# Optimization experiments

Measured on AMD Instinct MI355X. Metric: run time of the kernel, lower is better.

Reference implementation:

```python
import jax, jax.numpy as jnp
import numpy as np

N = 100000   # nodes
E = 1600000  # edges
F = 128      # input node features
H = 128      # hidden channels
G = 512      # graphs in batch
EPS = 1e-5   # BatchNorm eps


def setup_inputs() -> dict:
    key = jax.random.key(0)
    ks = jax.random.split(key, 24)
    x = jax.random.normal(ks[0], (N, F), jnp.float32)
    edge_index = jax.random.randint(ks[1], (2, E), 0, N)
    batch = jnp.sort(jax.random.randint(ks[2], (N,), 0, G))

    def lin_w(k, i, o):
        return jax.random.normal(k, (i, o), jnp.float32) / np.sqrt(i)

    inp = {
        "x": x, "edge_index": edge_index, "batch": batch,
        "W1": lin_w(ks[3], F, H), "b1": jnp.zeros((H,), jnp.float32),
        "g1": jnp.ones((H,), jnp.float32), "be1": jnp.zeros((H,), jnp.float32),
        "m1": 0.1 * jax.random.normal(ks[4], (H,), jnp.float32),
        "v1": jax.random.uniform(ks[5], (H,), jnp.float32) + 0.5,
        "W2": lin_w(ks[6], H, H), "b2": jnp.zeros((H,), jnp.float32),
        "g2": jnp.ones((H,), jnp.float32), "be2": jnp.zeros((H,), jnp.float32),
        "m2": 0.1 * jax.random.normal(ks[7], (H,), jnp.float32),
        "v2": jax.random.uniform(ks[8], (H,), jnp.float32) + 0.5,
        "W3": lin_w(ks[9], H, H), "b3": jnp.zeros((H,), jnp.float32),
        "g3": jnp.ones((H,), jnp.float32), "be3": jnp.zeros((H,), jnp.float32),
        "m3": 0.1 * jax.random.normal(ks[10], (H,), jnp.float32),
        "v3": jax.random.uniform(ks[11], (H,), jnp.float32) + 0.5,
        "Wl": lin_w(ks[12], H, 1), "bl": jnp.zeros((1,), jnp.float32),
    }
    return inp


def _gcn_norm(edge_index):
    # add self-loops, then symmetric normalization deg^-1/2 A_hat deg^-1/2
    loops = jnp.arange(N)
    src = jnp.concatenate([edge_index[0], loops])
    dst = jnp.concatenate([edge_index[1], loops])
    deg = jax.ops.segment_sum(jnp.ones_like(src, jnp.float32), dst, num_segments=N)
    dinv = jax.lax.rsqrt(jnp.maximum(deg, 1.0))
    norm = dinv[src] * dinv[dst]  # [E+N]
    return src, dst, norm


def _gcn_conv(x, W, b, src, dst, norm):
    h = x @ W                                    # [N,H] dense GEMM first (PyG order)
    msg = h[src] * norm[:, None]                 # gather + scale, [E+N,H]
    agg = jax.ops.segment_sum(msg, dst, num_segments=N)  # scatter-add
    return agg + b


def _bn_relu(x, g, be, m, v):
    # inference BatchNorm1d (running stats) + ReLU
    return jax.nn.relu((x - m) * jax.lax.rsqrt(v + EPS) * g + be)


def reference(x, edge_index, batch,
              W1, b1, g1, be1, m1, v1,
              W2, b2, g2, be2, m2, v2,
              W3, b3, g3, be3, m3, v3,
              Wl, bl):
    src, dst, norm = _gcn_norm(edge_index)
    h = _bn_relu(_gcn_conv(x, W1, b1, src, dst, norm), g1, be1, m1, v1)
    h = _bn_relu(_gcn_conv(h, W2, b2, src, dst, norm), g2, be2, m2, v2)
    h = _bn_relu(_gcn_conv(h, W3, b3, src, dst, norm), g3, be3, m3, v3)
    # global mean pool over graphs
    sums = jax.ops.segment_sum(h, batch, num_segments=G)           # [G,H]
    cnt = jax.ops.segment_sum(jnp.ones((N,), jnp.float32), batch, num_segments=G)
    pooled = sums / jnp.maximum(cnt, 1.0)[:, None]
    # dropout is identity at inference; final linear
    return pooled @ Wl + bl  # [G,1]
```

## Files before the change

kernel.cpp:

```cpp
#include <hip/hip_runtime.h>
#include <hip/hip_bf16.h>

#define NN 100000
#define NE 1600000
#define HD 128
#define NG 512
#define BN_EPS 1e-5f

#define GEMM_BLOCKS 1563

typedef __attribute__((ext_vector_type(8))) short short8;
typedef __attribute__((ext_vector_type(4))) float floatx4;

__device__ __forceinline__ ushort f2bf(float f) {
    union { float f; uint u; } v; v.f = f;
    uint r = (v.u + 0x7FFF + ((v.u >> 16) & 1)) >> 16;
    return (ushort)r;
}
__device__ __forceinline__ float bflo(uint u) { union { uint u; float f; } v; v.u = u << 16; return v.f; }
__device__ __forceinline__ float bfhi(uint u) { union { uint u; float f; } v; v.u = u & 0xFFFF0000u; return v.f; }

__global__ void k_zero_i(int* p, int n) {
    int i = blockIdx.x * 256 + threadIdx.x;
    if (i < n) p[i] = 0;
}

__global__ void k_prep_all(const float* __restrict__ W1, const float* __restrict__ W2,
                           const float* __restrict__ W3,
                           ushort* __restrict__ Wt1, ushort* __restrict__ Wt2,
                           ushort* __restrict__ Wt3,
                           const float* __restrict__ b1, const float* __restrict__ g1,
                           const float* __restrict__ be1, const float* __restrict__ m1,
                           const float* __restrict__ v1,
                           const float* __restrict__ b2, const float* __restrict__ g2,
                           const float* __restrict__ be2, const float* __restrict__ m2,
                           const float* __restrict__ v2,
                           const float* __restrict__ b3, const float* __restrict__ g3,
                           const float* __restrict__ be3, const float* __restrict__ m3,
                           const float* __restrict__ v3,
                           float* scale1, float* shift1, float* scale2, float* shift2,
                           float* scale3, float* shift3,
                           const int* __restrict__ batch, int* __restrict__ gstart) {
    int blk = blockIdx.x, tid = threadIdx.x;
    if (blk < 192) {
        int w = blk >> 6;
        int i = (blk & 63) * 256 + tid;
        const float* W = (w == 0) ? W1 : (w == 1) ? W2 : W3;
        ushort* Wt = (w == 0) ? Wt1 : (w == 1) ? Wt2 : Wt3;
        int k = i >> 7, n = i & 127;
        Wt[n * 128 + k] = f2bf(W[i]);
    } else if (blk < 195) {
        if (tid >= 128) return;
        int l = blk - 192;
        const float *b, *g, *be, *m, *v;
        float *sc, *sh;
        if (l == 0)      { b = b1; g = g1; be = be1; m = m1; v = v1; sc = scale1; sh = shift1; }
        else if (l == 1) { b = b2; g = g2; be = be2; m = m2; v = v2; sc = scale2; sh = shift2; }
        else             { b = b3; g = g3; be = be3; m = m3; v = v3; sc = scale3; sh = shift3; }
        float s = g[tid] * rsqrtf(v[tid] + BN_EPS);
        sc[tid] = s;
        sh[tid] = (b[tid] - m[tid]) * s + be[tid];
    } else {
        int g = (blk - 195) * 256 + tid;
        if (g > NG) return;
        if (g == NG) { gstart[NG] = NN; return; }
        int lo = 0, hi = NN;
        while (lo < hi) {
            int mid = (lo + hi) >> 1;
            if (batch[mid] < g) lo = mid + 1; else hi = mid;
        }
        gstart[g] = lo;
    }
}

__global__ void k_hist_rank(const int* __restrict__ dst, int* __restrict__ indeg,
                            int* __restrict__ rank) {
    int e = blockIdx.x * 256 + threadIdx.x;
    if (e < NE) rank[e] = atomicAdd(&indeg[dst[e]], 1);
}

__launch_bounds__(256)
__global__ void k_gemm1(const float* __restrict__ x, const ushort* __restrict__ Wt,
                        ushort* __restrict__ hs) {
    const int tid = threadIdx.x;
    const int wave = tid >> 6, lane = tid & 63;
    const int m = lane & 15, kg = lane >> 4;
    const long row0 = (long)blockIdx.x * 64 + wave * 16;

    long arow = row0 + m;
    long arc = arow < NN ? arow : (NN - 1);
    const float* xf = x + arc * 128;
    short8 a[4];
#pragma unroll
    for (int s = 0; s < 4; ++s) {
        float4 f0 = *(const float4*)(xf + s * 32 + kg * 8);
        float4 f1 = *(const float4*)(xf + s * 32 + kg * 8 + 4);
        short8 t;
        t[0] = (short)f2bf(f0.x); t[1] = (short)f2bf(f0.y);
        t[2] = (short)f2bf(f0.z); t[3] = (short)f2bf(f0.w);
        t[4] = (short)f2bf(f1.x); t[5] = (short)f2bf(f1.y);
        t[6] = (short)f2bf(f1.z); t[7] = (short)f2bf(f1.w);
        a[s] = t;
    }

    floatx4 acc[8];
#pragma unroll
    for (int ct = 0; ct < 8; ++ct) acc[ct] = (floatx4){0.f, 0.f, 0.f, 0.f};

#pragma unroll
    for (int s = 0; s < 4; ++s) {
#pragma unroll
        for (int ct = 0; ct < 8; ++ct) {
            short8 b = *(const short8*)(Wt + (ct * 16 + m) * 128 + s * 32 + kg * 8);
            acc[ct] = __builtin_amdgcn_mfma_f32_16x16x32_bf16(a[s], b, acc[ct], 0, 0, 0);
        }
    }

#pragma unroll
    for (int r = 0; r < 4; ++r) {
        long orow = row0 + kg * 4 + r;
        if (orow < NN) {
#pragma unroll
            for (int ct = 0; ct < 8; ++ct)
                hs[orow * 128 + ct * 16 + m] = f2bf(acc[ct][r]);
        }
    }
}

__global__ void k_scan1d(const int* __restrict__ indeg, int* __restrict__ rs,
                         int* __restrict__ aux, float* __restrict__ dinv) {
    __shared__ int s[256];
    int t = threadIdx.x;
    int base = blockIdx.x * 1024 + t * 4;
    int v0 = 0, v1 = 0, v2 = 0, v3 = 0;
    if (base + 0 < NN) v0 = indeg[base + 0];
    if (base + 1 < NN) v1 = indeg[base + 1];
    if (base + 2 < NN) v2 = indeg[base + 2];
    if (base + 3 < NN) v3 = indeg[base + 3];
    if (base + 0 < NN) dinv[base + 0] = rsqrtf((float)(v0 + 1));
    if (base + 1 < NN) dinv[base + 1] = rsqrtf((float)(v1 + 1));
    if (base + 2 < NN) dinv[base + 2] = rsqrtf((float)(v2 + 1));
    if (base + 3 < NN) dinv[base + 3] = rsqrtf((float)(v3 + 1));
    int tsum = v0 + v1 + v2 + v3;
    s[t] = tsum;
    __syncthreads();
    for (int o = 1; o < 256; o <<= 1) {
        int x = 0;
        if (t >= o) x = s[t - o];
        __syncthreads();
        s[t] += x;
        __syncthreads();
    }
    int excl = s[t] - tsum;
    if (base + 0 < NN) rs[base + 0] = excl;
    if (base + 1 < NN) rs[base + 1] = excl + v0;
    if (base + 2 < NN) rs[base + 2] = excl + v0 + v1;
    if (base + 3 < NN) rs[base + 3] = excl + v0 + v1 + v2;
    if (t == 255) aux[blockIdx.x] = s[255];
}

__global__ void k_scan2(int* __restrict__ aux, int nblk) {
    __shared__ int s[128];
    int t = threadIdx.x;
    int v = (t < nblk) ? aux[t] : 0;
    s[t] = v;
    __syncthreads();
    for (int o = 1; o < 128; o <<= 1) {
        int x = 0;
        if (t >= o) x = s[t - o];
        __syncthreads();
        s[t] += x;
        __syncthreads();
    }
    if (t < nblk) aux[t] = s[t] - v;
}

__global__ void k_scan3(int* __restrict__ rs, const int* __restrict__ aux) {
    int i = blockIdx.x * 256 + threadIdx.x;
    if (i < NN) rs[i] += aux[i >> 10];
    if (i == 0) rs[NN] = NE;
}

__global__ void k_fill(const int* __restrict__ src, const int* __restrict__ dst,
                       const int* __restrict__ rank, const int* __restrict__ rs,
                       int* __restrict__ csr) {
    int e = blockIdx.x * 256 + threadIdx.x;
    if (e >= NE) return;
    csr[rs[dst[e]] + rank[e]] = src[e];
}

#define WT_STRIDE 136
__launch_bounds__(256)
__global__ void k_gemm_l23(const ushort* __restrict__ xb, const ushort* __restrict__ Wt,
                           const float* __restrict__ dinv, ushort* __restrict__ hs) {
    __shared__ ushort sWt[128 * WT_STRIDE];
    const int tid = threadIdx.x;
    for (int i = tid; i < 2048; i += 256) {
        int row = i >> 4, seg = i & 15;
        *(uint4*)&sWt[row * WT_STRIDE + seg * 8] = *(const uint4*)(Wt + row * 128 + seg * 8);
    }
    __syncthreads();

    const int wave = tid >> 6, lane = tid & 63;
    const int m = lane & 15, kg = lane >> 4;
    const long row0 = (long)blockIdx.x * 64 + wave * 16;

    long arow = row0 + m;
    long arc = arow < NN ? arow : (NN - 1);
    short8 a[4];
#pragma unroll
    for (int s = 0; s < 4; ++s)
        a[s] = *(const short8*)(xb + arc * 128 + s * 32 + kg * 8);

    floatx4 acc[8];
#pragma unroll
    for (int ct = 0; ct < 8; ++ct) acc[ct] = (floatx4){0.f, 0.f, 0.f, 0.f};

#pragma unroll
    for (int s = 0; s < 4; ++s) {
#pragma unroll
        for (int ct = 0; ct < 8; ++ct) {
            short8 b = *(const short8*)&sWt[(ct * 16 + m) * WT_STRIDE + s * 32 + kg * 8];
            acc[ct] = __builtin_amdgcn_mfma_f32_16x16x32_bf16(a[s], b, acc[ct], 0, 0, 0);
        }
    }

#pragma unroll
    for (int r = 0; r < 4; ++r) {
        long orow = row0 + kg * 4 + r;
        if (orow < NN) {
            float dd = dinv[orow];
#pragma unroll
            for (int ct = 0; ct < 8; ++ct)
                hs[orow * 128 + ct * 16 + m] = f2bf(acc[ct][r] * dd);
        }
    }
}

template <bool SCALE_SRC>
__global__ void k_gather_bf(const ushort* __restrict__ hs, const int* __restrict__ rs,
                            const int* __restrict__ csr, const float* __restrict__ dinv,
                            const float* __restrict__ scale, const float* __restrict__ shift,
                            ushort* __restrict__ xout) {
    int t = blockIdx.x * 256 + threadIdx.x;
    int d = t >> 4;
    if (d >= NN) return;
    int lane = t & 15;
    int c0 = lane * 8;
    int e0 = rs[d], e1 = rs[d + 1];
    float dd = dinv[d];

    uint4 sv = *(const uint4*)(hs + (long)d * 128 + c0);
    float w = SCALE_SRC ? dd : 1.0f;
    float a0 = w * bflo(sv.x), a1 = w * bfhi(sv.x), a2 = w * bflo(sv.y), a3 = w * bfhi(sv.y);
    float a4 = w * bflo(sv.z), a5 = w * bfhi(sv.z), a6 = w * bflo(sv.w), a7 = w * bfhi(sv.w);

    int j = e0;
    for (; j + 1 < e1; j += 2) {
        int s0 = csr[j], s1 = csr[j + 1];
        uint4 v0 = *(const uint4*)(hs + (long)s0 * 128 + c0);
        uint4 v1 = *(const uint4*)(hs + (long)s1 * 128 + c0);
        if (SCALE_SRC) {
            float w0 = dinv[s0], w1 = dinv[s1];
            a0 += w0 * bflo(v0.x) + w1 * bflo(v1.x);
            a1 += w0 * bfhi(v0.x) + w1 * bfhi(v1.x);
            a2 += w0 * bflo(v0.y) + w1 * bflo(v1.y);
            a3 += w0 * bfhi(v0.y) + w1 * bfhi(v1.y);
            a4 += w0 * bflo(v0.z) + w1 * bflo(v1.z);
            a5 += w0 * bfhi(v0.z) + w1 * bfhi(v1.z);
            a6 += w0 * bflo(v0.w) + w1 * bflo(v1.w);
            a7 += w0 * bfhi(v0.w) + w1 * bfhi(v1.w);
        } else {
            a0 += bflo(v0.x) + bflo(v1.x); a1 += bfhi(v0.x) + bfhi(v1.x);
            a2 += bflo(v0.y) + bflo(v1.y); a3 += bfhi(v0.y) + bfhi(v1.y);
            a4 += bflo(v0.z) + bflo(v1.z); a5 += bfhi(v0.z) + bfhi(v1.z);
            a6 += bflo(v0.w) + bflo(v1.w); a7 += bfhi(v0.w) + bfhi(v1.w);
        }
    }
    if (j < e1) {
        int s0 = csr[j];
        uint4 v0 = *(const uint4*)(hs + (long)s0 * 128 + c0);
        float w0 = SCALE_SRC ? dinv[s0] : 1.0f;
        a0 += w0 * bflo(v0.x); a1 += w0 * bfhi(v0.x);
        a2 += w0 * bflo(v0.y); a3 += w0 * bfhi(v0.y);
        a4 += w0 * bflo(v0.z); a5 += w0 * bfhi(v0.z);
        a6 += w0 * bflo(v0.w); a7 += w0 * bfhi(v0.w);
    }

    float4 sca = *(const float4*)(scale + c0);
    float4 scb = *(const float4*)(scale + c0 + 4);
    float4 sha = *(const float4*)(shift + c0);
    float4 shb = *(const float4*)(shift + c0 + 4);
    float r0 = fmaxf(dd * a0 * sca.x + sha.x, 0.f);
    float r1 = fmaxf(dd * a1 * sca.y + sha.y, 0.f);
    float r2 = fmaxf(dd * a2 * sca.z + sha.z, 0.f);
    float r3 = fmaxf(dd * a3 * sca.w + sha.w, 0.f);
    float r4 = fmaxf(dd * a4 * scb.x + shb.x, 0.f);
    float r5 = fmaxf(dd * a5 * scb.y + shb.y, 0.f);
    float r6 = fmaxf(dd * a6 * scb.z + shb.z, 0.f);
    float r7 = fmaxf(dd * a7 * scb.w + shb.w, 0.f);
    uint4 o;
    o.x = (uint)f2bf(r0) | ((uint)f2bf(r1) << 16);
    o.y = (uint)f2bf(r2) | ((uint)f2bf(r3) << 16);
    o.z = (uint)f2bf(r4) | ((uint)f2bf(r5) << 16);
    o.w = (uint)f2bf(r6) | ((uint)f2bf(r7) << 16);
    *(uint4*)(xout + (long)d * 128 + c0) = o;
}

__global__ void k_pool_final2(const ushort* __restrict__ x, const int* __restrict__ gstart,
                              const float* __restrict__ Wl, const float* __restrict__ bl,
                              float* __restrict__ out) {
    __shared__ float red[256];
    int g = blockIdx.x;
    int tid = threadIdx.x;
    int f = tid & 127;
    int half = tid >> 7;
    int i0 = gstart[g], i1 = gstart[g + 1];

    float acc = 0.f;
    for (int i = i0 + half; i < i1; i += 2) {
        union { uint u; float f; } v; v.u = (uint)x[(long)i * 128 + f] << 16;
        acc += v.f;
    }
    red[tid] = acc;
    __syncthreads();
    if (tid < 128) red[tid] = (red[tid] + red[tid + 128]) * Wl[tid];
    __syncthreads();
    for (int o = 64; o > 0; o >>= 1) {
        if (tid < o) red[tid] += red[tid + o];
        __syncthreads();
    }
    if (tid == 0) out[g] = red[0] / fmaxf((float)(i1 - i0), 1.f) + bl[0];
}

extern "C" void kernel_launch(void* const* d_in, const int* in_sizes, int n_in,
                              void* d_out, int out_size, void* d_ws, size_t ws_size,
                              hipStream_t stream) {
    const float* x   = (const float*)d_in[0];
    const int*   ei  = (const int*)d_in[1];
    const int*   bat = (const int*)d_in[2];
    const float* W1  = (const float*)d_in[3];
    const float* b1  = (const float*)d_in[4];
    const float* g1  = (const float*)d_in[5];
    const float* be1 = (const float*)d_in[6];
    const float* m1  = (const float*)d_in[7];
    const float* v1  = (const float*)d_in[8];
    const float* W2  = (const float*)d_in[9];
    const float* b2  = (const float*)d_in[10];
    const float* g2  = (const float*)d_in[11];
    const float* be2 = (const float*)d_in[12];
    const float* m2  = (const float*)d_in[13];
    const float* v2  = (const float*)d_in[14];
    const float* W3  = (const float*)d_in[15];
    const float* b3  = (const float*)d_in[16];
    const float* g3  = (const float*)d_in[17];
    const float* be3 = (const float*)d_in[18];
    const float* m3  = (const float*)d_in[19];
    const float* v3  = (const float*)d_in[20];
    const float* Wl  = (const float*)d_in[21];
    const float* bl  = (const float*)d_in[22];
    float* out = (float*)d_out;

    const int* srcp = ei;
    const int* dstp = ei + NE;

    char* ws = (char*)d_ws;
    size_t off = 0;
    auto alloc = [&](size_t bytes) { char* p = ws + off; off += (bytes + 255) & ~255ULL; return p; };
    float*  dinv   = (float*) alloc(NN * 4);
    int*    indeg  = (int*)   alloc(NN * 4);
    int*    rs     = (int*)   alloc((NN + 1) * 4);
    int*    aux    = (int*)   alloc(128 * 4);
    int*    csr    = (int*)   alloc(NE * 4);
    int*    rank   = (int*)   alloc(NE * 4);
    float*  scale1 = (float*) alloc(HD * 4);
    float*  shift1 = (float*) alloc(HD * 4);
    float*  scale2 = (float*) alloc(HD * 4);
    float*  shift2 = (float*) alloc(HD * 4);
    float*  scale3 = (float*) alloc(HD * 4);
    float*  shift3 = (float*) alloc(HD * 4);
    int*    gstart = (int*)   alloc((NG + 1) * 4);
    ushort* Wt1    = (ushort*)alloc(128 * 128 * 2);
    ushort* Wt2    = (ushort*)alloc(128 * 128 * 2);
    ushort* Wt3    = (ushort*)alloc(128 * 128 * 2);
    ushort* hs     = (ushort*)alloc((size_t)NN * HD * 2);
    ushort* xbuf   = (ushort*)alloc((size_t)NN * HD * 2);

    const int nblk_scan = (NN + 1023) / 1024;
    const int grid_n    = (NN + 255) / 256;
    const int grid_e    = (NE + 255) / 256;
    const int gath_grid = (NN * 16 + 255) / 256;

    k_zero_i<<<grid_n, 256, 0, stream>>>(indeg, NN);
    k_prep_all<<<198, 256, 0, stream>>>(W1, W2, W3, Wt1, Wt2, Wt3,
                                        b1, g1, be1, m1, v1,
                                        b2, g2, be2, m2, v2,
                                        b3, g3, be3, m3, v3,
                                        scale1, shift1, scale2, shift2, scale3, shift3,
                                        bat, gstart);

    k_hist_rank<<<grid_e, 256, 0, stream>>>(dstp, indeg, rank);
    k_gemm1<<<GEMM_BLOCKS, 256, 0, stream>>>(x, Wt1, hs);

    k_scan1d<<<nblk_scan, 256, 0, stream>>>(indeg, rs, aux, dinv);
    k_scan2<<<1, 128, 0, stream>>>(aux, nblk_scan);
    k_scan3<<<grid_n, 256, 0, stream>>>(rs, aux);
    k_fill<<<grid_e, 256, 0, stream>>>(srcp, dstp, rank, rs, csr);

    k_gather_bf<true><<<gath_grid, 256, 0, stream>>>(hs, rs, csr, dinv, scale1, shift1, xbuf);
    k_gemm_l23<<<GEMM_BLOCKS, 256, 0, stream>>>(xbuf, Wt2, dinv, hs);
    k_gather_bf<false><<<gath_grid, 256, 0, stream>>>(hs, rs, csr, dinv, scale2, shift2, xbuf);
    k_gemm_l23<<<GEMM_BLOCKS, 256, 0, stream>>>(xbuf, Wt3, dinv, hs);
    k_gather_bf<false><<<gath_grid, 256, 0, stream>>>(hs, rs, csr, dinv, scale3, shift3, xbuf);

    k_pool_final2<<<NG, 256, 0, stream>>>(xbuf, gstart, Wl, bl, out);
}
```

Baseline: 520.0 us.

## Partition degree histogram by XCD with workgroup-scope atomics and chunk cursors

The in-degree histogram is restructured so that each XCD (read from the hardware XCC_ID register) owns a contiguous 1/8 range of destination nodes. Every XCD scans all edges through a per-XCD work-stealing chunk cursor and applies only the increments that fall in its range, using workgroup-scope atomics so they can resolve in the local L2 rather than going device-wide. The separate zeroing kernel is folded into the prep kernel, which saves one launch. In exchange each XCD reads the whole dst array (8x read traffic), and correctness depends on each XCD's L2 staying coherent for its own partition and on the assumption that blocks get scheduled onto all 8 XCDs.

```diff
diff --git a/kernel.cpp b/kernel.cpp
--- a/kernel.cpp
+++ b/kernel.cpp
@@ -8,6 +8,10 @@
 #define BN_EPS 1e-5f
 
 #define GEMM_BLOCKS 1563
+#define NXCD 8
+#define NODES_PER_XCD (NN / NXCD)
+#define CHUNK 4096
+#define NCHUNK ((NE + CHUNK - 1) / CHUNK)
 
 typedef __attribute__((ext_vector_type(8))) short short8;
 typedef __attribute__((ext_vector_type(4))) float floatx4;
@@ -20,9 +24,14 @@
 __device__ __forceinline__ float bflo(uint u) { union { uint u; float f; } v; v.u = u << 16; return v.f; }
 __device__ __forceinline__ float bfhi(uint u) { union { uint u; float f; } v; v.u = u & 0xFFFF0000u; return v.f; }
 
-__global__ void k_zero_i(int* p, int n) {
-    int i = blockIdx.x * 256 + threadIdx.x;
-    if (i < n) p[i] = 0;
+__device__ __forceinline__ uint xcc_id() {
+    uint x;
+    asm volatile("s_getreg_b32 %0, hwreg(HW_REG_XCC_ID)" : "=s"(x));
+    return x & 7u;
+}
+
+__device__ __forceinline__ int atomAddL2(int* p, int v) {
+    return __hip_atomic_fetch_add(p, v, __ATOMIC_RELAXED, __HIP_MEMORY_SCOPE_WORKGROUP);
 }
 
 __global__ void k_prep_all(const float* __restrict__ W1, const float* __restrict__ W2,
@@ -40,7 +49,8 @@
                            const float* __restrict__ v3,
                            float* scale1, float* shift1, float* scale2, float* shift2,
                            float* scale3, float* shift3,
-                           const int* __restrict__ batch, int* __restrict__ gstart) {
+                           const int* __restrict__ batch, int* __restrict__ gstart,
+                           int* __restrict__ indeg, int* __restrict__ cursor) {
     int blk = blockIdx.x, tid = threadIdx.x;
     if (blk < 192) {
         int w = blk >> 6;
@@ -60,7 +70,7 @@
         float s = g[tid] * rsqrtf(v[tid] + BN_EPS);
         sc[tid] = s;
         sh[tid] = (b[tid] - m[tid]) * s + be[tid];
-    } else {
+    } else if (blk < 198) {
         int g = (blk - 195) * 256 + tid;
         if (g > NG) return;
         if (g == NG) { gstart[NG] = NN; return; }
@@ -70,13 +80,48 @@
             if (batch[mid] < g) lo = mid + 1; else hi = mid;
         }
         gstart[g] = lo;
-    }
-}
-
-__global__ void k_hist_rank(const int* __restrict__ dst, int* __restrict__ indeg,
-                            int* __restrict__ rank) {
-    int e = blockIdx.x * 256 + threadIdx.x;
-    if (e < NE) rank[e] = atomicAdd(&indeg[dst[e]], 1);
+    } else {
+        int i = (blk - 198) * 256 + tid;
+        if (i < NN) indeg[i] = 0;
+        if (blk == 198 && tid < NXCD) cursor[tid] = 0;
+    }
+}
+
+__launch_bounds__(256)
+__global__ void k_hist_x(const int* __restrict__ dst, int* __restrict__ indeg,
+                         int* __restrict__ rank, int* __restrict__ cursor) {
+    __shared__ int sCur;
+    const int tid = threadIdx.x;
+    const uint xcc = xcc_id();
+    const int lo = (int)xcc * NODES_PER_XCD;
+    const int hi = lo + NODES_PER_XCD;
+
+    for (;;) {
+        if (tid == 0) sCur = atomicAdd(&cursor[xcc], 1);
+        __syncthreads();
+        int c = sCur;
+        __syncthreads();
+        if (c >= NCHUNK) break;
+        int base = c * CHUNK + tid * 16;
+        if (base + 16 <= NE) {
+#pragma unroll
+            for (int q = 0; q < 4; ++q) {
+                int4 dv = *(const int4*)(dst + base + q * 4);
+                int e = base + q * 4;
+                if (dv.x >= lo && dv.x < hi) rank[e]     = atomAddL2(&indeg[dv.x], 1);
+                if (dv.y >= lo && dv.y < hi) rank[e + 1] = atomAddL2(&indeg[dv.y], 1);
+                if (dv.z >= lo && dv.z < hi) rank[e + 2] = atomAddL2(&indeg[dv.z], 1);
+                if (dv.w >= lo && dv.w < hi) rank[e + 3] = atomAddL2(&indeg[dv.w], 1);
+            }
+        } else {
+            for (int q = 0; q < 16; ++q) {
+                int e = base + q;
+                if (e >= NE) break;
+                int d = dst[e];
+                if (d >= lo && d < hi) rank[e] = atomAddL2(&indeg[d], 1);
+            }
+        }
+    }
 }
 
 __launch_bounds__(256)
@@ -371,6 +416,7 @@
     int*    indeg  = (int*)   alloc(NN * 4);
     int*    rs     = (int*)   alloc((NN + 1) * 4);
     int*    aux    = (int*)   alloc(128 * 4);
+    int*    cursor = (int*)   alloc(NXCD * 4);
     int*    csr    = (int*)   alloc(NE * 4);
     int*    rank   = (int*)   alloc(NE * 4);
     float*  scale1 = (float*) alloc(HD * 4);
@@ -391,15 +437,14 @@
     const int grid_e    = (NE + 255) / 256;
     const int gath_grid = (NN * 16 + 255) / 256;
 
-    k_zero_i<<<grid_n, 256, 0, stream>>>(indeg, NN);
-    k_prep_all<<<198, 256, 0, stream>>>(W1, W2, W3, Wt1, Wt2, Wt3,
+    k_prep_all<<<589, 256, 0, stream>>>(W1, W2, W3, Wt1, Wt2, Wt3,
                                         b1, g1, be1, m1, v1,
                                         b2, g2, be2, m2, v2,
                                         b3, g3, be3, m3, v3,
                                         scale1, shift1, scale2, shift2, scale3, shift3,
-                                        bat, gstart);
-
-    k_hist_rank<<<grid_e, 256, 0, stream>>>(dstp, indeg, rank);
+                                        bat, gstart, indeg, cursor);
+
+    k_hist_x<<<2048, 256, 0, stream>>>(dstp, indeg, rank, cursor);
     k_gemm1<<<GEMM_BLOCKS, 256, 0, stream>>>(x, Wt1, hs);
 
     k_scan1d<<<nblk_scan, 256, 0, stream>>>(indeg, rs, aux, dinv);
```

Result: slower. 569.8 us (+9.6%).
